# Kernel tuning notes

Measured on AMD Instinct MI355X. Metric: run time of the kernel, lower is better.

## Reference

```python
import jax, jax.numpy as jnp
import numpy as np

D_MODEL = 1024
NHEAD = 16
D_HEAD = D_MODEL // NHEAD


def setup_inputs() -> dict:
    key = jax.random.key(0)
    ks = jax.random.split(key, 5)
    s_in = 1.0 / np.sqrt(D_MODEL)
    x = jax.random.normal(ks[0], (2, 2048, D_MODEL), dtype=jnp.float32)
    Wqkv = jax.random.uniform(ks[1], (D_MODEL, 3 * D_MODEL), jnp.float32, -s_in, s_in)
    bqkv = jax.random.uniform(ks[2], (3 * D_MODEL,), jnp.float32, -s_in, s_in)
    Wproj = jax.random.uniform(ks[3], (D_MODEL, D_MODEL), jnp.float32, -s_in, s_in)
    bproj = jax.random.uniform(ks[4], (D_MODEL,), jnp.float32, -s_in, s_in)
    return {"x": x, "Wqkv": Wqkv, "bqkv": bqkv, "Wproj": Wproj, "bproj": bproj}


def reference(x, Wqkv, bqkv, Wproj, bproj):
    B, N, D = x.shape
    qkv = x @ Wqkv + bqkv                       # [B, N, 3D]
    q, k, v = jnp.split(qkv, 3, axis=-1)
    # [B, N, D] -> [B, H, N, d]
    def to_heads(t):
        return t.reshape(B, N, NHEAD, D_HEAD).transpose(0, 2, 1, 3)
    q, k, v = to_heads(q), to_heads(k), to_heads(v)
    scale = 1.0 / np.sqrt(D_HEAD).astype(np.float32)
    attn = jnp.einsum('bhqd,bhkd->bhqk', q, k) * scale
    attn = jax.nn.softmax(attn, axis=-1)
    y = jnp.einsum('bhqk,bhkd->bhqd', attn, v)  # [B, H, N, d]
    y = y.transpose(0, 2, 1, 3).reshape(B, N, D)
    return y @ Wproj + bproj
```

## Files before the change

kernel.cpp:

```cpp
#include <hip/hip_runtime.h>
#include <hip/hip_bf16.h>
#include <stdint.h>

typedef __hip_bfloat16 bf16;
typedef __attribute__((ext_vector_type(8))) short short8;
typedef __attribute__((ext_vector_type(4))) float f32x4;

#define QSCALE 0.18033688011f

__device__ __forceinline__ float fast_exp2(float x) {
#if __has_builtin(__builtin_amdgcn_exp2f)
  return __builtin_amdgcn_exp2f(x);
#else
  return exp2f(x);
#endif
}

__device__ __forceinline__ uint32_t pack2_bf16(float a, float b) {
#if __has_builtin(__builtin_amdgcn_cvt_pk_bf16_f32)
  typedef __attribute__((ext_vector_type(2))) __bf16 bf16x2;
  bf16x2 v = __builtin_amdgcn_cvt_pk_bf16_f32(a, b);
  return __builtin_bit_cast(uint32_t, v);
#else
  uint32_t ua = __builtin_bit_cast(uint32_t, a);
  uint32_t ub = __builtin_bit_cast(uint32_t, b);
  ua += 0x7FFF + ((ua >> 16) & 1);
  ub += 0x7FFF + ((ub >> 16) & 1);
  return (ua >> 16) | (ub & 0xFFFF0000u);
#endif
}

__device__ __forceinline__ void gload_lds16(const bf16* g, bf16* l) {
#if __has_builtin(__builtin_amdgcn_global_load_lds)
  __builtin_amdgcn_global_load_lds(
      (const __attribute__((address_space(1))) void*)(uintptr_t)g,
      (__attribute__((address_space(3))) void*)(uint32_t)(uintptr_t)l,
      16, 0, 0);
#else
  int lane = threadIdx.x & 63;
  *(short8*)(l + lane * 8) = *(const short8*)(g + lane * 8);
#endif
}

__device__ __forceinline__ void lds_barrier() {
  asm volatile("s_waitcnt lgkmcnt(0)\n\ts_barrier" ::: "memory");
}

__device__ __forceinline__ void transpose_tile(const float* __restrict__ in,
                                               bf16* __restrict__ out,
                                               int R, int C, int bx, int by,
                                               bf16 (*t)[72]) {
  const int r0 = by * 64, c0 = bx * 64;
  const int rr = threadIdx.x >> 3, cc = (threadIdx.x & 7) * 8;
#pragma unroll
  for (int rep = 0; rep < 2; ++rep) {
    int y = rr + rep * 32;
    const float* p = in + (size_t)(r0 + y) * C + c0 + cc;
    f32x4 v0 = *(const f32x4*)p;
    f32x4 v1 = *(const f32x4*)(p + 4);
#pragma unroll
    for (int j = 0; j < 4; ++j) {
      t[cc + j][y] = __float2bfloat16(v0[j]);
      t[cc + 4 + j][y] = __float2bfloat16(v1[j]);
    }
  }
  __syncthreads();
#pragma unroll
  for (int rep = 0; rep < 2; ++rep) {
    int y = rr + rep * 32;
    short8 v = *(const short8*)&t[y][cc];
    *(short8*)(out + (size_t)(c0 + y) * R + r0 + cc) = v;
  }
}

__global__ __launch_bounds__(256)
void prep_k(const float* __restrict__ x, bf16* __restrict__ xb,
            const float* __restrict__ Wqkv, bf16* __restrict__ WtQkv,
            const float* __restrict__ Wproj, bf16* __restrict__ WtP) {
  __shared__ __align__(16) bf16 t[64][72];
  const int bid = blockIdx.x;
  if (bid < 2048) {
    int i = (bid * 256 + threadIdx.x) * 8;
    f32x4 v0 = *(const f32x4*)(x + i);
    f32x4 v1 = *(const f32x4*)(x + i + 4);
    short8 r;
    bf16* rb = (bf16*)&r;
#pragma unroll
    for (int j = 0; j < 4; ++j) {
      rb[j] = __float2bfloat16(v0[j]);
      rb[4 + j] = __float2bfloat16(v1[j]);
    }
    *(short8*)(xb + i) = r;
  } else if (bid < 2048 + 768) {
    int b = bid - 2048;
    transpose_tile(Wqkv, WtQkv, 1024, 3072, b % 48, b / 48, t);
  } else {
    int b = bid - 2816;
    transpose_tile(Wproj, WtP, 1024, 1024, b % 16, b / 16, t);
  }
}

template <int MODE, int TM>
__global__ __launch_bounds__(256, 2)
void gemm_bt(const bf16* __restrict__ A, const bf16* __restrict__ Bt,
             const float* __restrict__ bias, float* __restrict__ outp,
             bf16* __restrict__ Qd, bf16* __restrict__ Kd, bf16* __restrict__ Vt,
             int M, int Nn, int K) {
  constexpr int MI = TM / 32;
  __shared__ __align__(16) bf16 smem[(TM == 128) ? 9216 : 6144];
  bf16* As = smem;
  bf16* Bs = smem + TM * 32;

  const int tid = threadIdx.x;
  const int wave = tid >> 6, lane = tid & 63;
  const int quad = lane >> 4, l16 = lane & 15;
  const int mw = (wave >> 1) * (TM / 2), nw = (wave & 1) * 64;
  const int m_blk = blockIdx.y * TM, n_blk = blockIdx.x * 128;

  f32x4 acc[MI][4];
#pragma unroll
  for (int i = 0; i < MI; ++i)
#pragma unroll
    for (int j = 0; j < 4; ++j) acc[i][j] = (f32x4){0.f, 0.f, 0.f, 0.f};

  const int rowA = lane >> 2, colA = (lane & 3) * 8;
  const int chunkB = wave * 2;
  const bf16* gB = Bt + (size_t)(n_blk + chunkB * 16 + rowA) * K + colA;
  bf16* lB0 = &Bs[chunkB * 16 * 32];
  bf16* lB1 = &Bs[(chunkB + 1) * 16 * 32];

  const int chunkA = (TM == 128) ? wave * 2 : wave;
  const bf16* gA = A + (size_t)(m_blk + chunkA * 16 + rowA) * K + colA;
  bf16* lA0 = &As[chunkA * 16 * 32];
  bf16* lA1 = &As[(chunkA + 1) * 16 * 32];

  for (int kt = 0; kt < K; kt += 32) {
    gload_lds16(gA, lA0);
    if (TM == 128) gload_lds16(gA + 16 * K, lA1);
    gload_lds16(gB, lB0);
    gload_lds16(gB + 16 * K, lB1);
    gA += 32; gB += 32;
    __syncthreads();
    short8 af[MI], bfv[4];
#pragma unroll
    for (int i = 0; i < MI; ++i)
      af[i] = *(const short8*)&As[(mw + i * 16 + l16) * 32 + quad * 8];
#pragma unroll
    for (int j = 0; j < 4; ++j)
      bfv[j] = *(const short8*)&Bs[(nw + j * 16 + l16) * 32 + quad * 8];
#pragma unroll
    for (int i = 0; i < MI; ++i)
#pragma unroll
      for (int j = 0; j < 4; ++j)
        acc[i][j] = __builtin_amdgcn_mfma_f32_16x16x32_bf16(af[i], bfv[j],
                                                            acc[i][j], 0, 0, 0);
    __syncthreads();
  }

  if (MODE == 0) {
    float bval[4];
#pragma unroll
    for (int j = 0; j < 4; ++j) bval[j] = bias[n_blk + nw + j * 16 + l16];

    const int part = n_blk >> 10;
    const int b = m_blk >> 11;
    const int tloc = m_blk & 2047;
    const int h0 = (n_blk & 1023) >> 6;

#pragma unroll
    for (int p = 0; p < 2; ++p) {
      __syncthreads();
      if ((nw >> 6) == p) {
        if (part == 2) {
#pragma unroll
          for (int i = 0; i < MI; ++i)
#pragma unroll
            for (int j = 0; j < 4; ++j) {
              const int dh = j * 16 + l16;
              const int t0 = mw + i * 16 + quad * 4;
              uint2 pk;
              pk.x = pack2_bf16(acc[i][j][0] + bval[j], acc[i][j][1] + bval[j]);
              pk.y = pack2_bf16(acc[i][j][2] + bval[j], acc[i][j][3] + bval[j]);
              *(uint2*)&smem[dh * 136 + t0] = pk;
            }
        } else {
          const float sc = (part == 0) ? QSCALE : 1.0f;
#pragma unroll
          for (int i = 0; i < MI; ++i)
#pragma unroll
            for (int j = 0; j < 4; ++j) {
              const int d = j * 16 + l16;
              const int t0 = mw + i * 16 + quad * 4;
#pragma unroll
              for (int r = 0; r < 4; ++r)
                smem[(t0 + r) * 72 + d] =
                    __float2bfloat16((acc[i][j][r] + bval[j]) * sc);
            }
        }
      }
      __syncthreads();
      const size_t bh = (size_t)(b * 16 + h0 + p);
      if (part == 2) {
#pragma unroll
        for (int it = 0; it < 4; ++it) {
          const int dl = (tid >> 4) + it * 16;
          const int t8 = (tid & 15) * 8;
          short8 v = *(const short8*)&smem[dl * 136 + t8];
          *(short8*)&Vt[(bh * 64 + dl) * 2048 + tloc + t8] = v;
        }
      } else {
        bf16* dst = (part == 0) ? Qd : Kd;
#pragma unroll
        for (int it = 0; it < 4; ++it) {
          const int row = (tid >> 3) + it * 32;
          const int col8 = (tid & 7) * 8;
          short8 v = *(const short8*)&smem[row * 72 + col8];
          *(short8*)&dst[(bh * 2048 + tloc + row) * 64 + col8] = v;
        }
      }
    }
  } else {
#pragma unroll
    for (int j = 0; j < 4; ++j) {
      const int ncol = n_blk + nw + j * 16 + l16;
      const float bval = bias[ncol];
#pragma unroll
      for (int i = 0; i < MI; ++i) {
        const int mrow0 = m_blk + mw + i * 16 + quad * 4;
#pragma unroll
        for (int r = 0; r < 4; ++r)
          outp[(size_t)(mrow0 + r) * Nn + ncol] = acc[i][j][r] + bval;
      }
    }
  }
}

__global__ __launch_bounds__(256, 4)
void attn_kernel(const bf16* __restrict__ Qg, const bf16* __restrict__ Kg,
                 const bf16* __restrict__ Vt, bf16* __restrict__ yg) {
  __shared__ __align__(16) char pool[36864];
  bf16* KsB = (bf16*)pool;
  bf16* VtsB = (bf16*)(pool + 18432);

  const int tid = threadIdx.x;
  const int wave = tid >> 6, lane = tid & 63;
  const int quad = lane >> 4, l16 = lane & 15;
  const int qh = wave & 1, kvh = wave >> 1;

  const int bx = blockIdx.x;
  const int qt = bx & 31;
  const int bh = bx >> 5;

  const bf16* Qb = Qg + ((size_t)bh * 2048 + qt * 64) * 64;
  const bf16* Kb = Kg + (size_t)bh * 2048 * 64;
  const bf16* Vtb = Vt + (size_t)bh * 64 * 2048;

  short8 qf[2][2];
#pragma unroll
  for (int qblk = 0; qblk < 2; ++qblk)
#pragma unroll
    for (int ks = 0; ks < 2; ++ks)
      qf[qblk][ks] = *(const short8*)(
          Qb + (size_t)(qh * 32 + qblk * 16 + l16) * 64 + ks * 32 + quad * 8);

  const int kr = tid >> 3, kc = (tid & 7) * 8;
  const int vdd = tid & 63, vo = tid >> 6;
  const int voff0 = vdd * 72 + (((vo) + (vdd >> 3)) & 7) * 8;
  const int voff1 = vdd * 72 + (((vo + 4) + (vdd >> 3)) & 7) * 8;
  const bf16* Kp0 = Kb + (size_t)kr * 64 + kc;
  const bf16* Kp1 = Kb + (size_t)(kr + 32) * 64 + kc;
  const bf16* Vp0 = Vtb + (size_t)vdd * 2048 + vo * 8;
  const bf16* Vp1 = Vtb + (size_t)vdd * 2048 + (vo + 4) * 8;

  {
    short8 a = *(const short8*)Kp0;
    short8 b = *(const short8*)Kp1;
    short8 c = *(const short8*)Vp0;
    short8 d = *(const short8*)Vp1;
    *(short8*)(KsB + kr * 72 + kc) = a;
    *(short8*)(KsB + (kr + 32) * 72 + kc) = b;
    *(short8*)(VtsB + voff0) = c;
    *(short8*)(VtsB + voff1) = d;
  }
  short8 gk0 = *(const short8*)(Kp0 + (size_t)64 * 64);
  short8 gk1 = *(const short8*)(Kp1 + (size_t)64 * 64);
  short8 gv0 = *(const short8*)(Vp0 + 64);
  short8 gv1 = *(const short8*)(Vp1 + 64);
  __syncthreads();

  f32x4 yacc[2][4];
#pragma unroll
  for (int qblk = 0; qblk < 2; ++qblk)
#pragma unroll
    for (int dblk = 0; dblk < 4; ++dblk)
      yacc[qblk][dblk] = (f32x4){0.f, 0.f, 0.f, 0.f};
  float sum_l[2] = {0.f, 0.f};

  const int kfo = (kvh * 32 + l16) * 72 + quad * 8;
  int vbo[4][2];
#pragma unroll
  for (int dblk = 0; dblk < 4; ++dblk) {
    const int d = dblk * 16 + l16;
#pragma unroll
    for (int kvblk = 0; kvblk < 2; ++kvblk) {
      const int c = kvh * 4 + kvblk * 2 + (quad >> 1);
      vbo[dblk][kvblk] = d * 72 + ((c + (d >> 3)) & 7) * 8 + (quad & 1) * 4;
    }
  }

  for (int kt = 0; kt < 2048; kt += 64) {
    const int cur = (kt >> 6) & 1;
    bf16* KsC = KsB + cur * 4608;
    bf16* VtsC = VtsB + cur * 4608;

    if (kt + 64 < 2048) {
      bf16* KsN = KsB + (cur ^ 1) * 4608;
      bf16* VtsN = VtsB + (cur ^ 1) * 4608;
      *(short8*)(KsN + kr * 72 + kc) = gk0;
      *(short8*)(KsN + (kr + 32) * 72 + kc) = gk1;
      *(short8*)(VtsN + voff0) = gv0;
      *(short8*)(VtsN + voff1) = gv1;
      if (kt + 128 < 2048) {
        gk0 = *(const short8*)(Kp0 + (size_t)(kt + 128) * 64);
        gk1 = *(const short8*)(Kp1 + (size_t)(kt + 128) * 64);
        gv0 = *(const short8*)(Vp0 + kt + 128);
        gv1 = *(const short8*)(Vp1 + kt + 128);
      }
    }

    short8 kf[2][2];
#pragma unroll
    for (int kvblk = 0; kvblk < 2; ++kvblk)
#pragma unroll
      for (int ks = 0; ks < 2; ++ks)
        kf[kvblk][ks] =
            *(const short8*)(KsC + kfo + kvblk * 16 * 72 + ks * 32);

    short8 pa8[2];
#pragma unroll
    for (int qblk = 0; qblk < 2; ++qblk) {
      f32x4 s0 = (f32x4){0.f, 0.f, 0.f, 0.f};
      f32x4 s1 = (f32x4){0.f, 0.f, 0.f, 0.f};
      s0 = __builtin_amdgcn_mfma_f32_16x16x32_bf16(kf[0][0], qf[qblk][0], s0, 0, 0, 0);
      s0 = __builtin_amdgcn_mfma_f32_16x16x32_bf16(kf[0][1], qf[qblk][1], s0, 0, 0, 0);
      s1 = __builtin_amdgcn_mfma_f32_16x16x32_bf16(kf[1][0], qf[qblk][0], s1, 0, 0, 0);
      s1 = __builtin_amdgcn_mfma_f32_16x16x32_bf16(kf[1][1], qf[qblk][1], s1, 0, 0, 0);
      float p0 = fast_exp2(s0[0]), p1 = fast_exp2(s0[1]);
      float p2 = fast_exp2(s0[2]), p3 = fast_exp2(s0[3]);
      float p4 = fast_exp2(s1[0]), p5 = fast_exp2(s1[1]);
      float p6 = fast_exp2(s1[2]), p7 = fast_exp2(s1[3]);
      sum_l[qblk] += ((p0 + p1) + (p2 + p3)) + ((p4 + p5) + (p6 + p7));
      uint4 u;
      u.x = pack2_bf16(p0, p1);
      u.y = pack2_bf16(p2, p3);
      u.z = pack2_bf16(p4, p5);
      u.w = pack2_bf16(p6, p7);
      pa8[qblk] = __builtin_bit_cast(short8, u);
    }

#pragma unroll
    for (int dblk = 0; dblk < 4; ++dblk) {
      uint2 lo = *(const uint2*)(VtsC + vbo[dblk][0]);
      uint2 hi = *(const uint2*)(VtsC + vbo[dblk][1]);
      uint4 u;
      u.x = lo.x; u.y = lo.y; u.z = hi.x; u.w = hi.y;
      short8 vb8 = __builtin_bit_cast(short8, u);
      yacc[0][dblk] = __builtin_amdgcn_mfma_f32_16x16x32_bf16(
          pa8[0], vb8, yacc[0][dblk], 0, 0, 0);
      yacc[1][dblk] = __builtin_amdgcn_mfma_f32_16x16x32_bf16(
          pa8[1], vb8, yacc[1][dblk], 0, 0, 0);
    }

    lds_barrier();
  }

#pragma unroll
  for (int qblk = 0; qblk < 2; ++qblk) {
    sum_l[qblk] += __shfl_xor(sum_l[qblk], 16);
    sum_l[qblk] += __shfl_xor(sum_l[qblk], 32);
  }
  __syncthreads();
  float* red = (float*)pool;
  float* sred = (float*)(pool + 16384);
  if (kvh == 1) {
#pragma unroll
    for (int qblk = 0; qblk < 2; ++qblk) {
#pragma unroll
      for (int dblk = 0; dblk < 4; ++dblk) {
        const int f = (qh * 2 + qblk) * 4 + dblk;
        *(f32x4*)&red[(f * 64 + quad * 16 + l16) * 4] = yacc[qblk][dblk];
      }
      if (quad == 0) sred[(qh * 2 + qblk) * 16 + l16] = sum_l[qblk];
    }
  }
  __syncthreads();
  if (kvh == 0) {
    const int b = bh >> 4, h = bh & 15;
    const size_t rowbase = (size_t)b * 2048 + qt * 64;
#pragma unroll
    for (int qblk = 0; qblk < 2; ++qblk) {
      sum_l[qblk] += sred[(qh * 2 + qblk) * 16 + l16];
#pragma unroll
      for (int dblk = 0; dblk < 4; ++dblk) {
        const int f = (qh * 2 + qblk) * 4 + dblk;
        f32x4 o = *(const f32x4*)&red[(f * 64 + quad * 16 + l16) * 4];
#pragma unroll
        for (int r = 0; r < 4; ++r) yacc[qblk][dblk][r] += o[r];
      }
#pragma unroll
      for (int r = 0; r < 4; ++r) {
        const float lv = __shfl(sum_l[qblk], quad * 4 + r, 16);
        const float inv = 1.f / lv;
        const int rr = qh * 32 + qblk * 16 + quad * 4 + r;
#pragma unroll
        for (int dblk = 0; dblk < 4; ++dblk)
          yg[(rowbase + rr) * 1024 + h * 64 + dblk * 16 + l16] =
              __float2bfloat16(yacc[qblk][dblk][r] * inv);
      }
    }
  }
}

extern "C" void kernel_launch(void* const* d_in, const int* in_sizes, int n_in,
                              void* d_out, int out_size, void* d_ws, size_t ws_size,
                              hipStream_t stream) {
  const float* x = (const float*)d_in[0];
  const float* Wqkv = (const float*)d_in[1];
  const float* bqkv = (const float*)d_in[2];
  const float* Wproj = (const float*)d_in[3];
  const float* bproj = (const float*)d_in[4];
  float* out = (float*)d_out;

  if (ws_size < (size_t)40 * 1024 * 1024) return;

  char* ws = (char*)d_ws;
  bf16* xb    = (bf16*)(ws + 0);
  bf16* yd    = (bf16*)(ws + 0);
  bf16* WtQkv = (bf16*)(ws + 8388608);
  bf16* WtP   = (bf16*)(ws + 14680064);
  bf16* Qd    = (bf16*)(ws + 16777216);
  bf16* Kd    = (bf16*)(ws + 25165824);
  bf16* Vten  = (bf16*)(ws + 33554432);

  prep_k<<<3072, 256, 0, stream>>>(x, xb, Wqkv, WtQkv, Wproj, WtP);
  gemm_bt<0, 128><<<dim3(24, 32), 256, 0, stream>>>(
      xb, WtQkv, bqkv, nullptr, Qd, Kd, Vten, 4096, 3072, 1024);
  attn_kernel<<<dim3(1024), 256, 0, stream>>>(Qd, Kd, Vten, yd);
  gemm_bt<1, 64><<<dim3(8, 64), 256, 0, stream>>>(
      yd, WtP, bproj, out, nullptr, nullptr, nullptr, 4096, 1024, 1024);
}
```

Baseline: 194.8 us.

## Split KV tile across four waves with 128-key steps and MFMA row sums

The attention kernel now has each of the four waves process all 64 query rows over its own 32-key slice of a 128-key tile, instead of a 2x2 split of query and key halves. Each K/V fragment loaded from LDS is therefore reused across four query blocks, and there are half as many loop iterations and barriers. Softmax row sums are computed with an MFMA against a ones vector in place of scalar adds and shuffles. The cost is more LDS (about 70 KB) and more registers, so launch bounds drop to 2 blocks per SM, and the final reduction now merges three waves' partial results.

New measurement: 202.2 us. +3.8%, slower.

```diff
diff --git a/kernel.cpp b/kernel.cpp
--- a/kernel.cpp
+++ b/kernel.cpp
@@ -235,17 +235,16 @@
   }
 }
 
-__global__ __launch_bounds__(256, 4)
+__global__ __launch_bounds__(256, 2)
 void attn_kernel(const bf16* __restrict__ Qg, const bf16* __restrict__ Kg,
                  const bf16* __restrict__ Vt, bf16* __restrict__ yg) {
-  __shared__ __align__(16) char pool[36864];
+  __shared__ __align__(16) char pool[71680];
   bf16* KsB = (bf16*)pool;
-  bf16* VtsB = (bf16*)(pool + 18432);
+  bf16* VtsB = (bf16*)(pool + 36864);
 
   const int tid = threadIdx.x;
   const int wave = tid >> 6, lane = tid & 63;
   const int quad = lane >> 4, l16 = lane & 15;
-  const int qh = wave & 1, kvh = wave >> 1;
 
   const int bx = blockIdx.x;
   const int qt = bx & 31;
@@ -255,76 +254,90 @@
   const bf16* Kb = Kg + (size_t)bh * 2048 * 64;
   const bf16* Vtb = Vt + (size_t)bh * 64 * 2048;
 
-  short8 qf[2][2];
-#pragma unroll
-  for (int qblk = 0; qblk < 2; ++qblk)
+  short8 qf[4][2];
+#pragma unroll
+  for (int qblk = 0; qblk < 4; ++qblk)
 #pragma unroll
     for (int ks = 0; ks < 2; ++ks)
       qf[qblk][ks] = *(const short8*)(
-          Qb + (size_t)(qh * 32 + qblk * 16 + l16) * 64 + ks * 32 + quad * 8);
+          Qb + (size_t)(qblk * 16 + l16) * 64 + ks * 32 + quad * 8);
 
   const int kr = tid >> 3, kc = (tid & 7) * 8;
   const int vdd = tid & 63, vo = tid >> 6;
-  const int voff0 = vdd * 72 + (((vo) + (vdd >> 3)) & 7) * 8;
-  const int voff1 = vdd * 72 + (((vo + 4) + (vdd >> 3)) & 7) * 8;
-  const bf16* Kp0 = Kb + (size_t)kr * 64 + kc;
-  const bf16* Kp1 = Kb + (size_t)(kr + 32) * 64 + kc;
-  const bf16* Vp0 = Vtb + (size_t)vdd * 2048 + vo * 8;
-  const bf16* Vp1 = Vtb + (size_t)vdd * 2048 + (vo + 4) * 8;
-
-  {
-    short8 a = *(const short8*)Kp0;
-    short8 b = *(const short8*)Kp1;
-    short8 c = *(const short8*)Vp0;
-    short8 d = *(const short8*)Vp1;
-    *(short8*)(KsB + kr * 72 + kc) = a;
-    *(short8*)(KsB + (kr + 32) * 72 + kc) = b;
-    *(short8*)(VtsB + voff0) = c;
-    *(short8*)(VtsB + voff1) = d;
-  }
-  short8 gk0 = *(const short8*)(Kp0 + (size_t)64 * 64);
-  short8 gk1 = *(const short8*)(Kp1 + (size_t)64 * 64);
-  short8 gv0 = *(const short8*)(Vp0 + 64);
-  short8 gv1 = *(const short8*)(Vp1 + 64);
+  const bf16* Kp = Kb + (size_t)kr * 64 + kc;
+  const bf16* Vp = Vtb + (size_t)vdd * 2048 + vo * 8;
+  int vws[4];
+#pragma unroll
+  for (int j = 0; j < 4; ++j)
+    vws[j] = vdd * 136 + (((vo + 4 * j) + (vdd >> 3)) & 15) * 8;
+
+#pragma unroll
+  for (int j = 0; j < 4; ++j) {
+    short8 a = *(const short8*)(Kp + (size_t)(32 * j) * 64);
+    *(short8*)(KsB + (kr + 32 * j) * 72 + kc) = a;
+  }
+#pragma unroll
+  for (int j = 0; j < 4; ++j) {
+    short8 c = *(const short8*)(Vp + j * 32);
+    *(short8*)(VtsB + vws[j]) = c;
+  }
+  short8 gk[4], gv[4];
+#pragma unroll
+  for (int j = 0; j < 4; ++j)
+    gk[j] = *(const short8*)(Kp + (size_t)(128 + 32 * j) * 64);
+#pragma unroll
+  for (int j = 0; j < 4; ++j)
+    gv[j] = *(const short8*)(Vp + 128 + j * 32);
   __syncthreads();
 
-  f32x4 yacc[2][4];
-#pragma unroll
-  for (int qblk = 0; qblk < 2; ++qblk)
+  f32x4 yacc[4][4];
+#pragma unroll
+  for (int qblk = 0; qblk < 4; ++qblk)
 #pragma unroll
     for (int dblk = 0; dblk < 4; ++dblk)
       yacc[qblk][dblk] = (f32x4){0.f, 0.f, 0.f, 0.f};
-  float sum_l[2] = {0.f, 0.f};
-
-  const int kfo = (kvh * 32 + l16) * 72 + quad * 8;
+  f32x4 sum_acc[4];
+#pragma unroll
+  for (int qblk = 0; qblk < 4; ++qblk)
+    sum_acc[qblk] = (f32x4){0.f, 0.f, 0.f, 0.f};
+
+  uint4 ones_u;
+  ones_u.x = ones_u.y = ones_u.z = ones_u.w = 0x3F803F80u;
+  const short8 ones8 = __builtin_bit_cast(short8, ones_u);
+
+  const int kfo = (wave * 32 + l16) * 72 + quad * 8;
   int vbo[4][2];
 #pragma unroll
   for (int dblk = 0; dblk < 4; ++dblk) {
     const int d = dblk * 16 + l16;
 #pragma unroll
     for (int kvblk = 0; kvblk < 2; ++kvblk) {
-      const int c = kvh * 4 + kvblk * 2 + (quad >> 1);
-      vbo[dblk][kvblk] = d * 72 + ((c + (d >> 3)) & 7) * 8 + (quad & 1) * 4;
-    }
-  }
-
-  for (int kt = 0; kt < 2048; kt += 64) {
-    const int cur = (kt >> 6) & 1;
-    bf16* KsC = KsB + cur * 4608;
-    bf16* VtsC = VtsB + cur * 4608;
-
-    if (kt + 64 < 2048) {
-      bf16* KsN = KsB + (cur ^ 1) * 4608;
-      bf16* VtsN = VtsB + (cur ^ 1) * 4608;
-      *(short8*)(KsN + kr * 72 + kc) = gk0;
-      *(short8*)(KsN + (kr + 32) * 72 + kc) = gk1;
-      *(short8*)(VtsN + voff0) = gv0;
-      *(short8*)(VtsN + voff1) = gv1;
-      if (kt + 128 < 2048) {
-        gk0 = *(const short8*)(Kp0 + (size_t)(kt + 128) * 64);
-        gk1 = *(const short8*)(Kp1 + (size_t)(kt + 128) * 64);
-        gv0 = *(const short8*)(Vp0 + kt + 128);
-        gv1 = *(const short8*)(Vp1 + kt + 128);
+      const int c = wave * 4 + kvblk * 2 + (quad >> 1);
+      vbo[dblk][kvblk] = d * 136 + ((c + (d >> 3)) & 15) * 8 + (quad & 1) * 4;
+    }
+  }
+
+  for (int kt = 0; kt < 2048; kt += 128) {
+    const int cur = (kt >> 7) & 1;
+    bf16* KsC = KsB + cur * 9216;
+    bf16* VtsC = VtsB + cur * 8704;
+
+    if (kt + 128 < 2048) {
+      bf16* KsN = KsB + (cur ^ 1) * 9216;
+      bf16* VtsN = VtsB + (cur ^ 1) * 8704;
+#pragma unroll
+      for (int j = 0; j < 4; ++j)
+        *(short8*)(KsN + (kr + 32 * j) * 72 + kc) = gk[j];
+#pragma unroll
+      for (int j = 0; j < 4; ++j)
+        *(short8*)(VtsN + vws[j]) = gv[j];
+      if (kt + 256 < 2048) {
+#pragma unroll
+        for (int j = 0; j < 4; ++j)
+          gk[j] = *(const short8*)(Kp + (size_t)(kt + 256 + 32 * j) * 64);
+#pragma unroll
+        for (int j = 0; j < 4; ++j)
+          gv[j] = *(const short8*)(Vp + kt + 256 + j * 32);
       }
     }
 
@@ -335,10 +348,16 @@
       for (int ks = 0; ks < 2; ++ks)
         kf[kvblk][ks] =
             *(const short8*)(KsC + kfo + kvblk * 16 * 72 + ks * 32);
-
-    short8 pa8[2];
-#pragma unroll
-    for (int qblk = 0; qblk < 2; ++qblk) {
+    uint2 vlo[4], vhi[4];
+#pragma unroll
+    for (int dblk = 0; dblk < 4; ++dblk) {
+      vlo[dblk] = *(const uint2*)(VtsC + vbo[dblk][0]);
+      vhi[dblk] = *(const uint2*)(VtsC + vbo[dblk][1]);
+    }
+
+    short8 pa8[4];
+#pragma unroll
+    for (int qblk = 0; qblk < 4; ++qblk) {
       f32x4 s0 = (f32x4){0.f, 0.f, 0.f, 0.f};
       f32x4 s1 = (f32x4){0.f, 0.f, 0.f, 0.f};
       s0 = __builtin_amdgcn_mfma_f32_16x16x32_bf16(kf[0][0], qf[qblk][0], s0, 0, 0, 0);
@@ -349,69 +368,70 @@
       float p2 = fast_exp2(s0[2]), p3 = fast_exp2(s0[3]);
       float p4 = fast_exp2(s1[0]), p5 = fast_exp2(s1[1]);
       float p6 = fast_exp2(s1[2]), p7 = fast_exp2(s1[3]);
-      sum_l[qblk] += ((p0 + p1) + (p2 + p3)) + ((p4 + p5) + (p6 + p7));
       uint4 u;
       u.x = pack2_bf16(p0, p1);
       u.y = pack2_bf16(p2, p3);
       u.z = pack2_bf16(p4, p5);
       u.w = pack2_bf16(p6, p7);
       pa8[qblk] = __builtin_bit_cast(short8, u);
+      sum_acc[qblk] = __builtin_amdgcn_mfma_f32_16x16x32_bf16(
+          pa8[qblk], ones8, sum_acc[qblk], 0, 0, 0);
     }
 
 #pragma unroll
     for (int dblk = 0; dblk < 4; ++dblk) {
-      uint2 lo = *(const uint2*)(VtsC + vbo[dblk][0]);
-      uint2 hi = *(const uint2*)(VtsC + vbo[dblk][1]);
       uint4 u;
-      u.x = lo.x; u.y = lo.y; u.z = hi.x; u.w = hi.y;
+      u.x = vlo[dblk].x; u.y = vlo[dblk].y;
+      u.z = vhi[dblk].x; u.w = vhi[dblk].y;
       short8 vb8 = __builtin_bit_cast(short8, u);
-      yacc[0][dblk] = __builtin_amdgcn_mfma_f32_16x16x32_bf16(
-          pa8[0], vb8, yacc[0][dblk], 0, 0, 0);
-      yacc[1][dblk] = __builtin_amdgcn_mfma_f32_16x16x32_bf16(
-          pa8[1], vb8, yacc[1][dblk], 0, 0, 0);
+#pragma unroll
+      for (int qblk = 0; qblk < 4; ++qblk)
+        yacc[qblk][dblk] = __builtin_amdgcn_mfma_f32_16x16x32_bf16(
+            pa8[qblk], vb8, yacc[qblk][dblk], 0, 0, 0);
     }
 
     lds_barrier();
   }
 
-#pragma unroll
-  for (int qblk = 0; qblk < 2; ++qblk) {
-    sum_l[qblk] += __shfl_xor(sum_l[qblk], 16);
-    sum_l[qblk] += __shfl_xor(sum_l[qblk], 32);
-  }
   __syncthreads();
   float* red = (float*)pool;
-  float* sred = (float*)(pool + 16384);
-  if (kvh == 1) {
-#pragma unroll
-    for (int qblk = 0; qblk < 2; ++qblk) {
-#pragma unroll
-      for (int dblk = 0; dblk < 4; ++dblk) {
-        const int f = (qh * 2 + qblk) * 4 + dblk;
-        *(f32x4*)&red[(f * 64 + quad * 16 + l16) * 4] = yacc[qblk][dblk];
-      }
-      if (quad == 0) sred[(qh * 2 + qblk) * 16 + l16] = sum_l[qblk];
+  if (wave != 0) {
+    float* buf = red + (wave - 1) * 4160;
+#pragma unroll
+    for (int qblk = 0; qblk < 4; ++qblk) {
+#pragma unroll
+      for (int dblk = 0; dblk < 4; ++dblk)
+        *(f32x4*)&buf[((qblk * 4 + dblk) * 64 + lane) * 4] = yacc[qblk][dblk];
+      if (l16 == 0)
+        *(f32x4*)&buf[4096 + qblk * 16 + quad * 4] = sum_acc[qblk];
     }
   }
   __syncthreads();
-  if (kvh == 0) {
+  if (wave == 0) {
+#pragma unroll
+    for (int w = 0; w < 3; ++w) {
+      float* buf = red + w * 4160;
+#pragma unroll
+      for (int qblk = 0; qblk < 4; ++qblk) {
+        f32x4 sp = *(const f32x4*)&buf[4096 + qblk * 16 + quad * 4];
+#pragma unroll
+        for (int r = 0; r < 4; ++r) sum_acc[qblk][r] += sp[r];
+#pragma unroll
+        for (int dblk = 0; dblk < 4; ++dblk) {
+          f32x4 o = *(const f32x4*)&buf[((qblk * 4 + dblk) * 64 + lane) * 4];
+#pragma unroll
+          for (int r = 0; r < 4; ++r) yacc[qblk][dblk][r] += o[r];
+        }
+      }
+    }
     const int b = bh >> 4, h = bh & 15;
     const size_t rowbase = (size_t)b * 2048 + qt * 64;
 #pragma unroll
-    for (int qblk = 0; qblk < 2; ++qblk) {
-      sum_l[qblk] += sred[(qh * 2 + qblk) * 16 + l16];
-#pragma unroll
-      for (int dblk = 0; dblk < 4; ++dblk) {
-        const int f = (qh * 2 + qblk) * 4 + dblk;
-        f32x4 o = *(const f32x4*)&red[(f * 64 + quad * 16 + l16) * 4];
-#pragma unroll
-        for (int r = 0; r < 4; ++r) yacc[qblk][dblk][r] += o[r];
-      }
+    for (int qblk = 0; qblk < 4; ++qblk) {
 #pragma unroll
       for (int r = 0; r < 4; ++r) {
-        const float lv = __shfl(sum_l[qblk], quad * 4 + r, 16);
-        const float inv = 1.f / lv;
-        const int rr = qh * 32 + qblk * 16 + quad * 4 + r;
+        const float inv = 1.f / sum_acc[qblk][r];
+        const int rr = qblk * 16 + quad * 4 + r;
 #pragma unroll
         for (int dblk = 0; dblk < 4; ++dblk)
           yg[(rowbase + rr) * 1024 + h * 64 + dblk * 16 + l16] =
```

## Load K fragments directly from global, permute V layout, compute row sums via MFMA

Applied to the files above, without the earlier changes.

The attention kernel stops staging K through shared memory. Each wave now loads its K MFMA fragments straight from global memory into registers, prefetching the next tile while the current one is processed. V tiles are stored in a permuted LDS layout so each fragment is a single 16-byte read. The softmax row sums are computed with an extra MFMA against a ones vector instead of VALU adds and shuffles. This halves LDS use and cuts LDS traffic, which may allow more blocks per CU. In exchange, K is read redundantly from global/L2 by each wave, and two extra MFMAs are issued per iteration.

Result: slower. 229.5 us (+17.8%).

```diff
diff --git a/kernel.cpp b/kernel.cpp
--- a/kernel.cpp
+++ b/kernel.cpp
@@ -238,9 +238,8 @@
 __global__ __launch_bounds__(256, 4)
 void attn_kernel(const bf16* __restrict__ Qg, const bf16* __restrict__ Kg,
                  const bf16* __restrict__ Vt, bf16* __restrict__ yg) {
-  __shared__ __align__(16) char pool[36864];
-  bf16* KsB = (bf16*)pool;
-  bf16* VtsB = (bf16*)(pool + 18432);
+  __shared__ __align__(16) char pool[18432];
+  bf16* VtsB = (bf16*)pool;
 
   const int tid = threadIdx.x;
   const int wave = tid >> 6, lane = tid & 63;
@@ -263,29 +262,33 @@
       qf[qblk][ks] = *(const short8*)(
           Qb + (size_t)(qh * 32 + qblk * 16 + l16) * 64 + ks * 32 + quad * 8);
 
-  const int kr = tid >> 3, kc = (tid & 7) * 8;
   const int vdd = tid & 63, vo = tid >> 6;
-  const int voff0 = vdd * 72 + (((vo) + (vdd >> 3)) & 7) * 8;
-  const int voff1 = vdd * 72 + (((vo + 4) + (vdd >> 3)) & 7) * 8;
-  const bf16* Kp0 = Kb + (size_t)kr * 64 + kc;
-  const bf16* Kp1 = Kb + (size_t)(kr + 32) * 64 + kc;
-  const bf16* Vp0 = Vtb + (size_t)vdd * 2048 + vo * 8;
-  const bf16* Vp1 = Vtb + (size_t)vdd * 2048 + (vo + 4) * 8;
-
+  const bf16* Vp = Vtb + (size_t)vdd * 2048 + vo * 8;
+  const int bcol0 = ((vo >> 2) << 5) | ((vo & 1) << 4) | ((vo & 2) << 1);
+  const int vc1 = vo + 4;
+  const int bcol1 = ((vc1 >> 2) << 5) | ((vc1 & 1) << 4) | ((vc1 & 2) << 1);
+
+  const bf16* KpF = Kb + (size_t)(kvh * 32 + l16) * 64 + quad * 8;
+
+  short8 kf[2][2];
   {
-    short8 a = *(const short8*)Kp0;
-    short8 b = *(const short8*)Kp1;
-    short8 c = *(const short8*)Vp0;
-    short8 d = *(const short8*)Vp1;
-    *(short8*)(KsB + kr * 72 + kc) = a;
-    *(short8*)(KsB + (kr + 32) * 72 + kc) = b;
-    *(short8*)(VtsB + voff0) = c;
-    *(short8*)(VtsB + voff1) = d;
-  }
-  short8 gk0 = *(const short8*)(Kp0 + (size_t)64 * 64);
-  short8 gk1 = *(const short8*)(Kp1 + (size_t)64 * 64);
-  short8 gv0 = *(const short8*)(Vp0 + 64);
-  short8 gv1 = *(const short8*)(Vp1 + 64);
+    short8 c0 = *(const short8*)Vp;
+    short8 c1 = *(const short8*)(Vp + 32);
+    uint4 u0 = __builtin_bit_cast(uint4, c0);
+    uint4 u1 = __builtin_bit_cast(uint4, c1);
+    *(uint2*)(VtsB + vdd * 72 + bcol0) = (uint2){u0.x, u0.y};
+    *(uint2*)(VtsB + vdd * 72 + bcol0 + 8) = (uint2){u0.z, u0.w};
+    *(uint2*)(VtsB + vdd * 72 + bcol1) = (uint2){u1.x, u1.y};
+    *(uint2*)(VtsB + vdd * 72 + bcol1 + 8) = (uint2){u1.z, u1.w};
+  }
+  short8 gv0 = *(const short8*)(Vp + 64);
+  short8 gv1 = *(const short8*)(Vp + 96);
+#pragma unroll
+  for (int kvblk = 0; kvblk < 2; ++kvblk)
+#pragma unroll
+    for (int ks = 0; ks < 2; ++ks)
+      kf[kvblk][ks] =
+          *(const short8*)(KpF + (size_t)(kvblk * 16) * 64 + ks * 32);
   __syncthreads();
 
   f32x4 yacc[2][4];
@@ -294,91 +297,92 @@
 #pragma unroll
     for (int dblk = 0; dblk < 4; ++dblk)
       yacc[qblk][dblk] = (f32x4){0.f, 0.f, 0.f, 0.f};
-  float sum_l[2] = {0.f, 0.f};
-
-  const int kfo = (kvh * 32 + l16) * 72 + quad * 8;
-  int vbo[4][2];
-#pragma unroll
-  for (int dblk = 0; dblk < 4; ++dblk) {
-    const int d = dblk * 16 + l16;
-#pragma unroll
-    for (int kvblk = 0; kvblk < 2; ++kvblk) {
-      const int c = kvh * 4 + kvblk * 2 + (quad >> 1);
-      vbo[dblk][kvblk] = d * 72 + ((c + (d >> 3)) & 7) * 8 + (quad & 1) * 4;
-    }
-  }
+  f32x4 sum_acc[2];
+  sum_acc[0] = (f32x4){0.f, 0.f, 0.f, 0.f};
+  sum_acc[1] = (f32x4){0.f, 0.f, 0.f, 0.f};
+
+  uint4 ones_u;
+  ones_u.x = ones_u.y = ones_u.z = ones_u.w = 0x3F803F80u;
+  const short8 ones8 = __builtin_bit_cast(short8, ones_u);
+
+  int vro[4];
+#pragma unroll
+  for (int dblk = 0; dblk < 4; ++dblk)
+    vro[dblk] = (dblk * 16 + l16) * 72 + kvh * 32 + quad * 8;
 
   for (int kt = 0; kt < 2048; kt += 64) {
     const int cur = (kt >> 6) & 1;
-    bf16* KsC = KsB + cur * 4608;
     bf16* VtsC = VtsB + cur * 4608;
 
+    short8 vb8[4];
+#pragma unroll
+    for (int dblk = 0; dblk < 4; ++dblk)
+      vb8[dblk] = *(const short8*)(VtsC + vro[dblk]);
+
     if (kt + 64 < 2048) {
-      bf16* KsN = KsB + (cur ^ 1) * 4608;
       bf16* VtsN = VtsB + (cur ^ 1) * 4608;
-      *(short8*)(KsN + kr * 72 + kc) = gk0;
-      *(short8*)(KsN + (kr + 32) * 72 + kc) = gk1;
-      *(short8*)(VtsN + voff0) = gv0;
-      *(short8*)(VtsN + voff1) = gv1;
+      uint4 u0 = __builtin_bit_cast(uint4, gv0);
+      uint4 u1 = __builtin_bit_cast(uint4, gv1);
+      *(uint2*)(VtsN + vdd * 72 + bcol0) = (uint2){u0.x, u0.y};
+      *(uint2*)(VtsN + vdd * 72 + bcol0 + 8) = (uint2){u0.z, u0.w};
+      *(uint2*)(VtsN + vdd * 72 + bcol1) = (uint2){u1.x, u1.y};
+      *(uint2*)(VtsN + vdd * 72 + bcol1 + 8) = (uint2){u1.z, u1.w};
       if (kt + 128 < 2048) {
-        gk0 = *(const short8*)(Kp0 + (size_t)(kt + 128) * 64);
-        gk1 = *(const short8*)(Kp1 + (size_t)(kt + 128) * 64);
-        gv0 = *(const short8*)(Vp0 + kt + 128);
-        gv1 = *(const short8*)(Vp1 + kt + 128);
-      }
-    }
-
-    short8 kf[2][2];
-#pragma unroll
-    for (int kvblk = 0; kvblk < 2; ++kvblk)
-#pragma unroll
-      for (int ks = 0; ks < 2; ++ks)
-        kf[kvblk][ks] =
-            *(const short8*)(KsC + kfo + kvblk * 16 * 72 + ks * 32);
+        gv0 = *(const short8*)(Vp + kt + 128);
+        gv1 = *(const short8*)(Vp + kt + 128 + 32);
+      }
+    }
+
+    f32x4 s0[2], s1[2];
+#pragma unroll
+    for (int qblk = 0; qblk < 2; ++qblk) {
+      f32x4 a0 = (f32x4){0.f, 0.f, 0.f, 0.f};
+      f32x4 a1 = (f32x4){0.f, 0.f, 0.f, 0.f};
+      a0 = __builtin_amdgcn_mfma_f32_16x16x32_bf16(kf[0][0], qf[qblk][0], a0, 0, 0, 0);
+      a0 = __builtin_amdgcn_mfma_f32_16x16x32_bf16(kf[0][1], qf[qblk][1], a0, 0, 0, 0);
+      a1 = __builtin_amdgcn_mfma_f32_16x16x32_bf16(kf[1][0], qf[qblk][0], a1, 0, 0, 0);
+      a1 = __builtin_amdgcn_mfma_f32_16x16x32_bf16(kf[1][1], qf[qblk][1], a1, 0, 0, 0);
+      s0[qblk] = a0;
+      s1[qblk] = a1;
+    }
+    if (kt + 64 < 2048) {
+      const bf16* kp = KpF + (size_t)(kt + 64) * 64;
+#pragma unroll
+      for (int kvblk = 0; kvblk < 2; ++kvblk)
+#pragma unroll
+        for (int ks = 0; ks < 2; ++ks)
+          kf[kvblk][ks] =
+              *(const short8*)(kp + (size_t)(kvblk * 16) * 64 + ks * 32);
+    }
 
     short8 pa8[2];
 #pragma unroll
     for (int qblk = 0; qblk < 2; ++qblk) {
-      f32x4 s0 = (f32x4){0.f, 0.f, 0.f, 0.f};
-      f32x4 s1 = (f32x4){0.f, 0.f, 0.f, 0.f};
-      s0 = __builtin_amdgcn_mfma_f32_16x16x32_bf16(kf[0][0], qf[qblk][0], s0, 0, 0, 0);
-      s0 = __builtin_amdgcn_mfma_f32_16x16x32_bf16(kf[0][1], qf[qblk][1], s0, 0, 0, 0);
-      s1 = __builtin_amdgcn_mfma_f32_16x16x32_bf16(kf[1][0], qf[qblk][0], s1, 0, 0, 0);
-      s1 = __builtin_amdgcn_mfma_f32_16x16x32_bf16(kf[1][1], qf[qblk][1], s1, 0, 0, 0);
-      float p0 = fast_exp2(s0[0]), p1 = fast_exp2(s0[1]);
-      float p2 = fast_exp2(s0[2]), p3 = fast_exp2(s0[3]);
-      float p4 = fast_exp2(s1[0]), p5 = fast_exp2(s1[1]);
-      float p6 = fast_exp2(s1[2]), p7 = fast_exp2(s1[3]);
-      sum_l[qblk] += ((p0 + p1) + (p2 + p3)) + ((p4 + p5) + (p6 + p7));
+      float p0 = fast_exp2(s0[qblk][0]), p1 = fast_exp2(s0[qblk][1]);
+      float p2 = fast_exp2(s0[qblk][2]), p3 = fast_exp2(s0[qblk][3]);
+      float p4 = fast_exp2(s1[qblk][0]), p5 = fast_exp2(s1[qblk][1]);
+      float p6 = fast_exp2(s1[qblk][2]), p7 = fast_exp2(s1[qblk][3]);
       uint4 u;
       u.x = pack2_bf16(p0, p1);
       u.y = pack2_bf16(p2, p3);
       u.z = pack2_bf16(p4, p5);
       u.w = pack2_bf16(p6, p7);
       pa8[qblk] = __builtin_bit_cast(short8, u);
+      sum_acc[qblk] = __builtin_amdgcn_mfma_f32_16x16x32_bf16(
+          pa8[qblk], ones8, sum_acc[qblk], 0, 0, 0);
     }
 
 #pragma unroll
     for (int dblk = 0; dblk < 4; ++dblk) {
-      uint2 lo = *(const uint2*)(VtsC + vbo[dblk][0]);
-      uint2 hi = *(const uint2*)(VtsC + vbo[dblk][1]);
-      uint4 u;
-      u.x = lo.x; u.y = lo.y; u.z = hi.x; u.w = hi.y;
-      short8 vb8 = __builtin_bit_cast(short8, u);
       yacc[0][dblk] = __builtin_amdgcn_mfma_f32_16x16x32_bf16(
-          pa8[0], vb8, yacc[0][dblk], 0, 0, 0);
+          pa8[0], vb8[dblk], yacc[0][dblk], 0, 0, 0);
       yacc[1][dblk] = __builtin_amdgcn_mfma_f32_16x16x32_bf16(
-          pa8[1], vb8, yacc[1][dblk], 0, 0, 0);
+          pa8[1], vb8[dblk], yacc[1][dblk], 0, 0, 0);
     }
 
     lds_barrier();
   }
 
-#pragma unroll
-  for (int qblk = 0; qblk < 2; ++qblk) {
-    sum_l[qblk] += __shfl_xor(sum_l[qblk], 16);
-    sum_l[qblk] += __shfl_xor(sum_l[qblk], 32);
-  }
   __syncthreads();
   float* red = (float*)pool;
   float* sred = (float*)(pool + 16384);
@@ -390,7 +394,8 @@
         const int f = (qh * 2 + qblk) * 4 + dblk;
         *(f32x4*)&red[(f * 64 + quad * 16 + l16) * 4] = yacc[qblk][dblk];
       }
-      if (quad == 0) sred[(qh * 2 + qblk) * 16 + l16] = sum_l[qblk];
+      if (l16 == 0)
+        *(f32x4*)&sred[(qh * 2 + qblk) * 16 + quad * 4] = sum_acc[qblk];
     }
   }
   __syncthreads();
@@ -399,7 +404,7 @@
     const size_t rowbase = (size_t)b * 2048 + qt * 64;
 #pragma unroll
     for (int qblk = 0; qblk < 2; ++qblk) {
-      sum_l[qblk] += sred[(qh * 2 + qblk) * 16 + l16];
+      f32x4 sp = *(const f32x4*)&sred[(qh * 2 + qblk) * 16 + quad * 4];
 #pragma unroll
       for (int dblk = 0; dblk < 4; ++dblk) {
         const int f = (qh * 2 + qblk) * 4 + dblk;
@@ -409,8 +414,7 @@
       }
 #pragma unroll
       for (int r = 0; r < 4; ++r) {
-        const float lv = __shfl(sum_l[qblk], quad * 4 + r, 16);
-        const float inv = 1.f / lv;
+        const float inv = 1.f / (sum_acc[qblk][r] + sp[r]);
         const int rr = qh * 32 + qblk * 16 + quad * 4 + r;
 #pragma unroll
         for (int dblk = 0; dblk < 4; ++dblk)
```

## Swizzle workgroup order for XCD locality and compute softmax sums via MFMA

Applied to the files above, without the earlier changes.

Remaps block indices in the GEMM and attention kernels so that consecutive blocks, which the hardware spreads round-robin across the 8 XCDs, land on the same XCD and share its L2 cache. In attention, the per-row exp sum is now computed with an extra MFMA against a vector of bf16 ones instead of scalar adds and cross-lane shuffles. This removes VALU work and shuffles from the inner loop but adds MFMA work. The sum now uses the bf16-rounded probabilities, which matches the values used for P·V. The GEMM swizzle assumes the grid size is divisible by 8.

Result: no change. 192.4 us (-1.2%).

```diff
diff --git a/kernel.cpp b/kernel.cpp
--- a/kernel.cpp
+++ b/kernel.cpp
@@ -115,7 +115,11 @@
   const int wave = tid >> 6, lane = tid & 63;
   const int quad = lane >> 4, l16 = lane & 15;
   const int mw = (wave >> 1) * (TM / 2), nw = (wave & 1) * 64;
-  const int m_blk = blockIdx.y * TM, n_blk = blockIdx.x * 128;
+
+  const int nwg = gridDim.x * gridDim.y;
+  const int ord = blockIdx.y * gridDim.x + blockIdx.x;
+  const int wg = (ord & 7) * (nwg >> 3) + (ord >> 3);
+  const int m_blk = (wg / gridDim.x) * TM, n_blk = (wg % gridDim.x) * 128;
 
   f32x4 acc[MI][4];
 #pragma unroll
@@ -247,7 +251,8 @@
   const int quad = lane >> 4, l16 = lane & 15;
   const int qh = wave & 1, kvh = wave >> 1;
 
-  const int bx = blockIdx.x;
+  const int bx0 = blockIdx.x;
+  const int bx = ((bx0 & 7) << 7) | (bx0 >> 3);
   const int qt = bx & 31;
   const int bh = bx >> 5;
 
@@ -294,7 +299,13 @@
 #pragma unroll
     for (int dblk = 0; dblk < 4; ++dblk)
       yacc[qblk][dblk] = (f32x4){0.f, 0.f, 0.f, 0.f};
-  float sum_l[2] = {0.f, 0.f};
+  f32x4 sum_acc[2];
+  sum_acc[0] = (f32x4){0.f, 0.f, 0.f, 0.f};
+  sum_acc[1] = (f32x4){0.f, 0.f, 0.f, 0.f};
+
+  uint4 ones_u;
+  ones_u.x = ones_u.y = ones_u.z = ones_u.w = 0x3F803F80u;
+  const short8 ones8 = __builtin_bit_cast(short8, ones_u);
 
   const int kfo = (kvh * 32 + l16) * 72 + quad * 8;
   int vbo[4][2];
@@ -349,13 +360,14 @@
       float p2 = fast_exp2(s0[2]), p3 = fast_exp2(s0[3]);
       float p4 = fast_exp2(s1[0]), p5 = fast_exp2(s1[1]);
       float p6 = fast_exp2(s1[2]), p7 = fast_exp2(s1[3]);
-      sum_l[qblk] += ((p0 + p1) + (p2 + p3)) + ((p4 + p5) + (p6 + p7));
       uint4 u;
       u.x = pack2_bf16(p0, p1);
       u.y = pack2_bf16(p2, p3);
       u.z = pack2_bf16(p4, p5);
       u.w = pack2_bf16(p6, p7);
       pa8[qblk] = __builtin_bit_cast(short8, u);
+      sum_acc[qblk] = __builtin_amdgcn_mfma_f32_16x16x32_bf16(
+          pa8[qblk], ones8, sum_acc[qblk], 0, 0, 0);
     }
 
 #pragma unroll
@@ -374,11 +386,6 @@
     lds_barrier();
   }
 
-#pragma unroll
-  for (int qblk = 0; qblk < 2; ++qblk) {
-    sum_l[qblk] += __shfl_xor(sum_l[qblk], 16);
-    sum_l[qblk] += __shfl_xor(sum_l[qblk], 32);
-  }
   __syncthreads();
   float* red = (float*)pool;
   float* sred = (float*)(pool + 16384);
@@ -390,7 +397,8 @@
         const int f = (qh * 2 + qblk) * 4 + dblk;
         *(f32x4*)&red[(f * 64 + quad * 16 + l16) * 4] = yacc[qblk][dblk];
       }
-      if (quad == 0) sred[(qh * 2 + qblk) * 16 + l16] = sum_l[qblk];
+      if (l16 == 0)
+        *(f32x4*)&sred[(qh * 2 + qblk) * 16 + quad * 4] = sum_acc[qblk];
     }
   }
   __syncthreads();
@@ -399,7 +407,7 @@
     const size_t rowbase = (size_t)b * 2048 + qt * 64;
 #pragma unroll
     for (int qblk = 0; qblk < 2; ++qblk) {
-      sum_l[qblk] += sred[(qh * 2 + qblk) * 16 + l16];
+      f32x4 sp = *(const f32x4*)&sred[(qh * 2 + qblk) * 16 + quad * 4];
 #pragma unroll
       for (int dblk = 0; dblk < 4; ++dblk) {
         const int f = (qh * 2 + qblk) * 4 + dblk;
@@ -409,8 +417,7 @@
       }
 #pragma unroll
       for (int r = 0; r < 4; ++r) {
-        const float lv = __shfl(sum_l[qblk], quad * 4 + r, 16);
-        const float inv = 1.f / lv;
+        const float inv = 1.f / (sum_acc[qblk][r] + sp[r]);
         const int rr = qh * 32 + qblk * 16 + quad * 4 + r;
 #pragma unroll
         for (int dblk = 0; dblk < 4; ++dblk)
```
